# Performance work log

Hardware: AMD Instinct MI355X
Metric: run time of the kernel (lower is better)

## Reference

```python
import jax
import jax.numpy as jnp
import numpy as np
from jax import lax

SURROGATE_SCALE = 10.0  # SuperSpike slope parameter

@jax.custom_vjp
def spike_fn(u):
    # Heaviside forward: spike if membrane potential exceeds threshold
    return (u > 0).astype(u.dtype)

def _spike_fwd(u):
    return spike_fn(u), u

def _spike_bwd(u, g):
    # SuperSpike surrogate gradient: 1 / (scale*|u| + 1)^2
    sg = 1.0 / jnp.square(SURROGATE_SCALE * jnp.abs(u) + 1.0)
    return (g * sg,)

spike_fn.defvjp(_spike_fwd, _spike_bwd)

B, C, T = 64, 512, 1024

def setup_inputs() -> dict:
    key = jax.random.key(0)
    k1, k2 = jax.random.split(key)
    x = jax.random.normal(k1, (B, C, T), dtype=jnp.float32)
    # scalar trainable leak (torch init: normal(0.7, 0.01) clamped to [0,1])
    beta = jnp.clip(0.7 + 0.01 * jax.random.normal(k2, (), dtype=jnp.float32), 0.0, 1.0)
    vth = jnp.ones((C,), dtype=jnp.float32)  # non-trainable threshold
    return {"x": x, "beta": beta, "vth": vth}

def reference(x, beta, vth):
    # x: (B, C, T), time_position=2, negative_mempot=True, flatten_output=False
    b, c, t = x.shape
    xt = jnp.moveaxis(x, 2, 0)  # (T, B, C)

    def step(carry, inp):
        mem, spk = carry
        rst = spk * vth                 # einsum('ab,b->ab', spk, Vth)
        mem = mem * beta + inp - rst    # negative_mempot branch
        spk = spike_fn(mem - vth)
        return (mem, spk), spk

    init = (jnp.zeros((b, c), x.dtype), jnp.zeros((b, c), x.dtype))
    _, spk_rec = lax.scan(step, init, xt)  # (T, B, C)
    return jnp.moveaxis(spk_rec, 0, 2)     # (B, C, T)
```

## Files before the change

kernel.cpp:

```cpp
#include <hip/hip_runtime.h>


typedef float f32x4 __attribute__((ext_vector_type(4)));

#define T_LEN   1024
#define C_LEN   512
#define RPB     64
#define CHUNK   64
#define VECS    16
#define NCH     (T_LEN / CHUNK)
#define ROWV    (T_LEN / 4)

#define STEP(xv_, sv_)                                 \
    do {                                               \
        float m1_ = __fmul_rn(mem, beta);              \
        float m2_ = __fadd_rn(m1_, (xv_));             \
        mem = __fsub_rn(m2_, rst);                     \
        bool b_ = (mem > vth);                         \
        (sv_) = b_ ? 1.0f : 0.0f;                      \
        rst = b_ ? vth : 0.0f;                         \
    } while (0)

#define LOADS(ch)                                                         \
    do {                                                                  \
        _Pragma("unroll")                                                 \
        for (int j_ = 0; j_ < VECS; ++j_) {                               \
            const int rj_ = 4 * j_ + l4;                                  \
            const int gc_ = c16 ^ (rj_ & 15);                             \
            stg[j_] = xv[(size_t)(rb + rj_) * ROWV + (ch) * VECS + gc_];  \
        }                                                                 \
    } while (0)

#define DSW(buf)                                                          \
    do {                                                                  \
        _Pragma("unroll")                                                 \
        for (int j_ = 0; j_ < VECS; ++j_)                                 \
            in_lds[buf][64 * j_ + l] = stg[j_];                           \
    } while (0)

#define COMPUTE(buf)                                                      \
    do {                                                                  \
        _Pragma("unroll")                                                 \
        for (int j_ = 0; j_ < VECS; ++j_) {                               \
            f32x4 v_ = in_lds[buf][l * VECS + (j_ ^ c16)];                \
            f32x4 s_;                                                     \
            STEP(v_.x, s_.x);                                             \
            STEP(v_.y, s_.y);                                             \
            STEP(v_.z, s_.z);                                             \
            STEP(v_.w, s_.w);                                             \
            out_lds[l * VECS + (j_ ^ c16)] = s_;                          \
        }                                                                 \
    } while (0)

#define DRAIN(ch)                                                         \
    do {                                                                  \
        _Pragma("unroll")                                                 \
        for (int j_ = 0; j_ < VECS; ++j_) {                               \
            const int rj_ = 4 * j_ + l4;                                  \
            const int gc_ = c16 ^ (rj_ & 15);                             \
            ov[(size_t)(rb + rj_) * ROWV + (ch) * VECS + gc_] =           \
                out_lds[64 * j_ + l];                                     \
        }                                                                 \
    } while (0)

__global__ __launch_bounds__(64, 1) void elif_scan_kernel(
    const float* __restrict__ x,
    const float* __restrict__ beta_p,
    const float* __restrict__ vth_p,
    float* __restrict__ out)
{
    __shared__ f32x4 in_lds[2][RPB * VECS];
    __shared__ f32x4 out_lds[RPB * VECS];

    const int l   = threadIdx.x;
    const int l4  = l >> 4;
    const int c16 = l & 15;
    const int rb  = blockIdx.x * RPB;

    const f32x4* __restrict__ xv = (const f32x4*)x;
    f32x4* __restrict__       ov = (f32x4*)out;

    const float beta = beta_p[0];
    const float vth  = vth_p[(rb + l) & (C_LEN - 1)];

    f32x4 stg[VECS];
    float mem = 0.0f;
    float rst = 0.0f;

    LOADS(0);
    DSW(0);
    LOADS(1);

    #pragma unroll 1
    for (int ch = 0; ch < NCH; ++ch) {
        COMPUTE(ch & 1);
        DRAIN(ch);
        if (ch < NCH - 1) DSW((ch + 1) & 1);
        if (ch < NCH - 2) LOADS(ch + 2);
    }
}

extern "C" void kernel_launch(void* const* d_in, const int* in_sizes, int n_in,
                              void* d_out, int out_size, void* d_ws, size_t ws_size,
                              hipStream_t stream) {
    const float* x      = (const float*)d_in[0];
    const float* beta_p = (const float*)d_in[1];
    const float* vth_p  = (const float*)d_in[2];
    float* out          = (float*)d_out;

    const int n_rows = in_sizes[0] / T_LEN;
    const int grid   = n_rows / RPB;

    elif_scan_kernel<<<grid, RPB, 0, stream>>>(x, beta_p, vth_p, out);
}
```

Baseline: 47.32 us.

## Load input chunks directly into LDS with triple-buffered global_load_lds pipeline

```diff
diff --git a/kernel.cpp b/kernel.cpp
--- a/kernel.cpp
+++ b/kernel.cpp
@@ -3,13 +3,19 @@
 
 typedef float f32x4 __attribute__((ext_vector_type(4)));
 
-#define T_LEN   1024
-#define C_LEN   512
-#define RPB     64
-#define CHUNK   64
-#define VECS    16
-#define NCH     (T_LEN / CHUNK)
-#define ROWV    (T_LEN / 4)
+#define T_LEN 1024
+#define C_LEN 512
+#define RPB   64
+#define VECS  16
+#define NCH   (T_LEN / (VECS * 4))
+#define ROWV  (T_LEN / 4)
+
+#define GLL(g_, l_)                                                     \
+    __builtin_amdgcn_global_load_lds(                                   \
+        (const __attribute__((address_space(1))) void*)(g_),            \
+        (__attribute__((address_space(3))) void*)(l_), 16, 0, 0)
+
+#define WAITV(n_) asm volatile("s_waitcnt vmcnt(" #n_ ")" ::: "memory")
 
 #define STEP(xv_, sv_)                                 \
     do {                                               \
@@ -21,21 +27,15 @@
         rst = b_ ? vth : 0.0f;                         \
     } while (0)
 
-#define LOADS(ch)                                                         \
-    do {                                                                  \
-        _Pragma("unroll")                                                 \
-        for (int j_ = 0; j_ < VECS; ++j_) {                               \
-            const int rj_ = 4 * j_ + l4;                                  \
-            const int gc_ = c16 ^ (rj_ & 15);                             \
-            stg[j_] = xv[(size_t)(rb + rj_) * ROWV + (ch) * VECS + gc_];  \
-        }                                                                 \
-    } while (0)
-
-#define DSW(buf)                                                          \
-    do {                                                                  \
-        _Pragma("unroll")                                                 \
-        for (int j_ = 0; j_ < VECS; ++j_)                                 \
-            in_lds[buf][64 * j_ + l] = stg[j_];                           \
+#define LOADS(buf, ch)                                                        \
+    do {                                                                      \
+        _Pragma("unroll")                                                     \
+        for (int j_ = 0; j_ < VECS; ++j_) {                                   \
+            const int rj_ = 4 * j_ + l4;                                      \
+            const int gc_ = c16 ^ (rj_ & 15);                                 \
+            GLL(xv + (size_t)(rb + rj_) * ROWV + (ch) * VECS + gc_,           \
+                &in_lds[buf][64 * j_]);                                       \
+        }                                                                     \
     } while (0)
 
 #define COMPUTE(buf)                                                      \
@@ -69,7 +69,7 @@
     const float* __restrict__ vth_p,
     float* __restrict__ out)
 {
-    __shared__ f32x4 in_lds[2][RPB * VECS];
+    __shared__ f32x4 in_lds[3][RPB * VECS];
     __shared__ f32x4 out_lds[RPB * VECS];
 
     const int l   = threadIdx.x;
@@ -83,20 +83,23 @@
     const float beta = beta_p[0];
     const float vth  = vth_p[(rb + l) & (C_LEN - 1)];
 
-    f32x4 stg[VECS];
     float mem = 0.0f;
     float rst = 0.0f;
 
-    LOADS(0);
-    DSW(0);
-    LOADS(1);
+    LOADS(0, 0);
+    LOADS(1, 1);
+
+    WAITV(16);
+    COMPUTE(0);
+    LOADS(2, 2);
+    DRAIN(0);
 
     #pragma unroll 1
-    for (int ch = 0; ch < NCH; ++ch) {
-        COMPUTE(ch & 1);
+    for (int ch = 1; ch < NCH; ++ch) {
+        WAITV(32);
+        COMPUTE(ch % 3);
+        if (ch + 2 < NCH) LOADS((ch + 2) % 3, ch + 2);
         DRAIN(ch);
-        if (ch < NCH - 1) DSW((ch + 1) & 1);
-        if (ch < NCH - 2) LOADS(ch + 2);
     }
 }
 
```

Result: slower. 53.06 us (+12.1%).
